# Kernel tuning notes

Measured on AMD Instinct MI355X. Metric: run time of the kernel, lower is better.

Reference implementation:

```python
import jax, jax.numpy as jnp
import numpy as np

HEADS = 8
DIM_HEAD = 64
DIM_INNER = HEADS * DIM_HEAD  # 512
SCALE = DIM_HEAD ** -0.5
B, N, D = 8, 512, 512
NEG = -1e9


def setup_inputs() -> dict:
    key = jax.random.key(0)
    ks = jax.random.split(key, 12)
    inp = {}
    for i in range(3):
        inp[f"x{i}"] = jax.random.normal(ks[i], (B, N, D), dtype=jnp.float32)
        inp[f"m{i}"] = jax.random.randint(ks[3 + i], (B, N), 0, 2).astype(bool)
        inp[f"Wqkv{i}"] = jax.random.normal(ks[6 + i], (D, 3 * DIM_INNER), dtype=jnp.float32) * 0.02
        inp[f"Wout{i}"] = jax.random.normal(ks[9 + i], (DIM_INNER, D), dtype=jnp.float32) * 0.02
    return inp


def _split_heads(t):
    # [b, n, h*d] -> [b, h, n, d]
    b, n, _ = t.shape
    return t.reshape(b, n, HEADS, DIM_HEAD).transpose(0, 2, 1, 3)


def _forward(xs, masks, Wqkvs, Wouts):
    qs, ks, vs = [], [], []
    for x, W in zip(xs, Wqkvs):
        q, k, v = jnp.split(x @ W, 3, axis=-1)
        qs.append(_split_heads(q))
        ks.append(_split_heads(k))
        vs.append(_split_heads(v))
    K = jnp.concatenate(ks, axis=2)  # [b, h, 3n, d]
    V = jnp.concatenate(vs, axis=2)
    outs = []
    for q, m, Wo in zip(qs, masks, Wouts):
        dots = jnp.einsum('bhnd,bhmd->bhnm', q, K) * SCALE
        # original masks whole query rows: masked_fill(~mask[:, None, :, None], -1e9)
        dots = jnp.where(m[:, None, :, None], dots, NEG)
        attn = jax.nn.softmax(dots, axis=-1)  # dropout is identity at eval
        o = jnp.einsum('bhnm,bhmd->bhnd', attn, V)
        o = o.transpose(0, 2, 1, 3).reshape(q.shape[0], q.shape[2], DIM_INNER)
        outs.append(o @ Wo)
    return tuple(outs)


def reference(x0, x1, x2, m0, m1, m2, Wqkv0, Wqkv1, Wqkv2, Wout0, Wout1, Wout2):
    return _forward((x0, x1, x2), (m0, m1, m2), (Wqkv0, Wqkv1, Wqkv2), (Wout0, Wout1, Wout2))
```

## Files before the change

kernel.cpp:

```cpp
#include <hip/hip_runtime.h>
#include <cstdint>
#include <cstddef>

#define NEGV  -1.0e9f
#define QSCALE 0.18033688011112042f

typedef _Float16 h8 __attribute__((ext_vector_type(8)));
typedef _Float16 h4 __attribute__((ext_vector_type(4)));
typedef float    f4 __attribute__((ext_vector_type(4)));


static __device__ inline h8 cvt8(float4 a, float4 b) {
    h8 r = { (_Float16)a.x, (_Float16)a.y, (_Float16)a.z, (_Float16)a.w,
             (_Float16)b.x, (_Float16)b.y, (_Float16)b.z, (_Float16)b.w };
    return r;
}

__global__ __launch_bounds__(256) void wt_cvt(
    const float* __restrict__ q0, const float* __restrict__ q1, const float* __restrict__ q2,
    const float* __restrict__ o0, const float* __restrict__ o1, const float* __restrict__ o2,
    _Float16* __restrict__ Wqt, _Float16* __restrict__ Wot)
{
    const int mod = blockIdx.z;
    const int flat = blockIdx.x;
    const float* s;
    _Float16* d;
    int C, bx, by;
    if (flat < 768) {
        C = 1536; bx = flat % 48; by = flat / 48;
        s = (mod == 0) ? q0 : ((mod == 1) ? q1 : q2);
        d = Wqt + (size_t)mod * 1536 * 512;
    } else {
        C = 512; bx = (flat - 768) % 16; by = (flat - 768) / 16;
        s = (mod == 0) ? o0 : ((mod == 1) ? o1 : o2);
        d = Wot + (size_t)mod * 512 * 512;
    }
    const int c0 = bx * 32, r0 = by * 32;
    __shared__ float tile[32][33];
    const int tr = threadIdx.x >> 3;
    const int tc = (threadIdx.x & 7) * 4;
    float4 v = *reinterpret_cast<const float4*>(&s[(size_t)(r0 + tr) * C + c0 + tc]);
    tile[tr][tc + 0] = v.x; tile[tr][tc + 1] = v.y; tile[tr][tc + 2] = v.z; tile[tr][tc + 3] = v.w;
    __syncthreads();
    h4 o = { (_Float16)tile[tc + 0][tr], (_Float16)tile[tc + 1][tr],
             (_Float16)tile[tc + 2][tr], (_Float16)tile[tc + 3][tr] };
    *reinterpret_cast<h4*>(&d[(size_t)(c0 + tr) * 512 + r0 + tc]) = o;
}

__global__ __launch_bounds__(256) void qkv_gemm_f16(
    const float* __restrict__ x0, const float* __restrict__ x1, const float* __restrict__ x2,
    const _Float16* __restrict__ Wqt,
    _Float16* __restrict__ Qh, _Float16* __restrict__ Kh, _Float16* __restrict__ Vt)
{
    const int mod = blockIdx.z;
    const float* __restrict__ A = (mod == 0) ? x0 : ((mod == 1) ? x1 : x2);
    const _Float16* __restrict__ Bw = Wqt + (size_t)mod * 1536 * 512;

    __shared__ _Float16 smem[2 * 128 * 72];
    _Float16* As = smem;
    _Float16* Bs = smem + 128 * 72;

    const int t = threadIdx.x;
    const int brow = blockIdx.x * 128, bcol = blockIdx.y * 128;
    const int w = t >> 6, l = t & 63;
    const int wr = (w >> 1) * 64, wc = (w & 1) * 64;
    const int lr = l & 15, lg = l >> 4, lk = lg * 8;

    const int sm = t >> 1, sk = (t & 1) * 32;
    const float*    __restrict__ aRow = &A [(size_t)(brow + sm) * 512 + sk];
    const _Float16* __restrict__ bRow = &Bw[(size_t)(bcol + sm) * 512 + sk];
    _Float16* aDst = &As[sm * 72 + sk];
    _Float16* bDst = &Bs[sm * 72 + sk];

    f4 acc[4][4] = {};
    float4 ax[8];
    h8 bx[4];

#pragma unroll
    for (int j = 0; j < 8; j++) ax[j] = *reinterpret_cast<const float4*>(&aRow[j * 4]);
#pragma unroll
    for (int j = 0; j < 4; j++) bx[j] = *reinterpret_cast<const h8*>(&bRow[j * 8]);
#pragma unroll
    for (int j = 0; j < 4; j++) {
        *reinterpret_cast<h8*>(&aDst[j * 8]) = cvt8(ax[2 * j], ax[2 * j + 1]);
        *reinterpret_cast<h8*>(&bDst[j * 8]) = bx[j];
    }

    for (int k0 = 0; k0 < 512; k0 += 64) {
        __syncthreads();
        const bool more = (k0 + 64) < 512;
        if (more) {
            const int kn = k0 + 64;
#pragma unroll
            for (int j = 0; j < 8; j++) ax[j] = *reinterpret_cast<const float4*>(&aRow[kn + j * 4]);
#pragma unroll
            for (int j = 0; j < 4; j++) bx[j] = *reinterpret_cast<const h8*>(&bRow[kn + j * 8]);
        }
#pragma unroll
        for (int ks = 0; ks < 64; ks += 32) {
            h8 af[4], bf[4];
#pragma unroll
            for (int m = 0; m < 4; m++)
                af[m] = *reinterpret_cast<h8*>(&As[(wr + m * 16 + lr) * 72 + ks + lk]);
#pragma unroll
            for (int n = 0; n < 4; n++)
                bf[n] = *reinterpret_cast<h8*>(&Bs[(wc + n * 16 + lr) * 72 + ks + lk]);
            __builtin_amdgcn_s_setprio(1);
#pragma unroll
            for (int m = 0; m < 4; m++)
#pragma unroll
                for (int n = 0; n < 4; n++)
                    acc[m][n] = __builtin_amdgcn_mfma_f32_16x16x32_f16(af[m], bf[n], acc[m][n], 0, 0, 0);
            __builtin_amdgcn_s_setprio(0);
        }
        __syncthreads();
        if (more) {
#pragma unroll
            for (int j = 0; j < 4; j++) {
                *reinterpret_cast<h8*>(&aDst[j * 8]) = cvt8(ax[2 * j], ax[2 * j + 1]);
                *reinterpret_cast<h8*>(&bDst[j * 8]) = bx[j];
            }
        }
    }

    const int sec = bcol >> 9;
    const int b = brow >> 9;
    const int nbase = brow & 511;
    const int cbase = bcol - (sec << 9);

    if (sec == 2) {
#pragma unroll
        for (int m = 0; m < 4; m++) {
            const int n = nbase + wr + m * 16 + lg * 4;
#pragma unroll
            for (int nn = 0; nn < 4; nn++) {
                const int cis = cbase + wc + nn * 16 + lr;
                const int hh = cis >> 6, d = cis & 63;
                h4 pv = { (_Float16)acc[m][nn][0], (_Float16)acc[m][nn][1],
                          (_Float16)acc[m][nn][2], (_Float16)acc[m][nn][3] };
                *reinterpret_cast<h4*>(&Vt[(((size_t)b * 8 + hh) * 64 + d) * 1536 + mod * 512 + n]) = pv;
            }
        }
    } else {
        const float scl = (sec == 0) ? QSCALE : 1.0f;
        _Float16 (*Ts)[136] = reinterpret_cast<_Float16(*)[136]>(smem);
#pragma unroll
        for (int pass = 0; pass < 2; pass++) {
            __syncthreads();
            if ((w >> 1) == pass) {
#pragma unroll
                for (int m = 0; m < 4; m++)
#pragma unroll
                    for (int nn = 0; nn < 4; nn++)
#pragma unroll
                        for (int reg = 0; reg < 4; reg++)
                            Ts[m * 16 + lg * 4 + reg][wc + nn * 16 + lr] =
                                (_Float16)(acc[m][nn][reg] * scl);
            }
            __syncthreads();
#pragma unroll
            for (int it = 0; it < 4; it++) {
                const int idx = t + it * 256;
                const int r = idx >> 4, c = (idx & 15) * 8;
                h8 v = *reinterpret_cast<h8*>(&Ts[r][c]);
                const int n = nbase + pass * 64 + r;
                const int cis = cbase + c;
                const int hh = cis >> 6, d = cis & 63;
                if (sec == 0)
                    *reinterpret_cast<h8*>(&Qh[((((size_t)mod * 8 + b) * 8 + hh) * 512 + n) * 64 + d]) = v;
                else
                    *reinterpret_cast<h8*>(&Kh[(((size_t)b * 8 + hh) * 1536 + mod * 512 + n) * 64 + d]) = v;
            }
        }
    }
}

__global__ __launch_bounds__(512) void attn_f16(
    const _Float16* __restrict__ Qh, const _Float16* __restrict__ Kh, const _Float16* __restrict__ Vt,
    const int* __restrict__ m0, const int* __restrict__ m1, const int* __restrict__ m2,
    _Float16* __restrict__ Oh)
{
    const int mod = blockIdx.z;
    const int bh = blockIdx.x, b = bh >> 3, h = bh & 7;
    const int q0 = blockIdx.y * 128;

    __shared__ _Float16 Ks[64 * 72];
    __shared__ _Float16 Vs[64 * 72];
    __shared__ _Float16 Ps[128 * 72];

    const int t = threadIdx.x, w = t >> 6, l = t & 63;
    const int lr = l & 15, lg = l >> 4, lk = lg * 8;

    const _Float16* __restrict__ Qp = Qh + ((((size_t)mod * 8 + b) * 8 + h) * 512 + q0 + w * 16) * 64;
    h8 qf0 = *reinterpret_cast<const h8*>(&Qp[(size_t)lr * 64 + lk]);
    h8 qf1 = *reinterpret_cast<const h8*>(&Qp[(size_t)lr * 64 + 32 + lk]);

    const int* __restrict__ mk = (mod == 0) ? m0 : ((mod == 1) ? m1 : m2);
    const bool msk = mk[b * 512 + q0 + w * 16 + lr] != 0;

    float mrow = -3.0e38f, lsum = 0.f;
    f4 o[4] = {};

    const int sr = t >> 3, skk = (t & 7) * 8;
    const _Float16* __restrict__ kSrc = Kh + (size_t)bh * 1536 * 64 + (size_t)sr * 64 + skk;
    const _Float16* __restrict__ vSrc = Vt + (size_t)bh * 64 * 1536 + (size_t)sr * 1536 + skk;
    _Float16* kDst = &Ks[sr * 72 + skk];
    _Float16* vDst = &Vs[sr * 72 + skk];

    h8 krg = *reinterpret_cast<const h8*>(kSrc);
    h8 vrg = *reinterpret_cast<const h8*>(vSrc);
    *reinterpret_cast<h8*>(kDst) = krg;
    *reinterpret_cast<h8*>(vDst) = vrg;

    for (int c0 = 0; c0 < 1536; c0 += 64) {
        __syncthreads();
        const bool more = (c0 + 64) < 1536;
        if (more) {
            krg = *reinterpret_cast<const h8*>(kSrc + (size_t)(c0 + 64) * 64);
            vrg = *reinterpret_cast<const h8*>(vSrc + (c0 + 64));
        }

        f4 st[4] = {};
        __builtin_amdgcn_s_setprio(1);
#pragma unroll
        for (int kb = 0; kb < 4; kb++) {
            h8 ka0 = *reinterpret_cast<h8*>(&Ks[(kb * 16 + lr) * 72 + lk]);
            h8 ka1 = *reinterpret_cast<h8*>(&Ks[(kb * 16 + lr) * 72 + 32 + lk]);
            st[kb] = __builtin_amdgcn_mfma_f32_16x16x32_f16(ka0, qf0, st[kb], 0, 0, 0);
            st[kb] = __builtin_amdgcn_mfma_f32_16x16x32_f16(ka1, qf1, st[kb], 0, 0, 0);
        }
        __builtin_amdgcn_s_setprio(0);

        if (!msk) {
#pragma unroll
            for (int kb = 0; kb < 4; kb++) { st[kb][0] = NEGV; st[kb][1] = NEGV; st[kb][2] = NEGV; st[kb][3] = NEGV; }
        }
        float cm = fmaxf(fmaxf(fmaxf(st[0][0], st[0][1]), fmaxf(st[0][2], st[0][3])),
                         fmaxf(fmaxf(st[1][0], st[1][1]), fmaxf(st[1][2], st[1][3])));
        cm = fmaxf(cm, fmaxf(fmaxf(fmaxf(st[2][0], st[2][1]), fmaxf(st[2][2], st[2][3])),
                             fmaxf(fmaxf(st[3][0], st[3][1]), fmaxf(st[3][2], st[3][3]))));
        cm = fmaxf(cm, __shfl_xor(cm, 16));
        cm = fmaxf(cm, __shfl_xor(cm, 32));

        if (!__all(cm <= mrow + 8.0f)) {
            const float mn = fmaxf(mrow, cm);
            const float sc = __builtin_amdgcn_exp2f(mrow - mn);
            mrow = mn;
            lsum *= sc;
#pragma unroll
            for (int dg = 0; dg < 4; dg++) o[dg] *= sc;
        }

        float rs = 0.f;
#pragma unroll
        for (int kb = 0; kb < 4; kb++) {
            const float p0 = __builtin_amdgcn_exp2f(st[kb][0] - mrow);
            const float p1 = __builtin_amdgcn_exp2f(st[kb][1] - mrow);
            const float p2 = __builtin_amdgcn_exp2f(st[kb][2] - mrow);
            const float p3 = __builtin_amdgcn_exp2f(st[kb][3] - mrow);
            rs += (p0 + p1) + (p2 + p3);
            h4 ph = { (_Float16)p0, (_Float16)p1, (_Float16)p2, (_Float16)p3 };
            *reinterpret_cast<h4*>(&Ps[(w * 16 + lr) * 72 + kb * 16 + lg * 4]) = ph;
        }
        rs += __shfl_xor(rs, 16);
        rs += __shfl_xor(rs, 32);
        lsum += rs;

        __builtin_amdgcn_s_setprio(1);
#pragma unroll
        for (int kb2 = 0; kb2 < 2; kb2++) {
            h8 pa = *reinterpret_cast<h8*>(&Ps[(w * 16 + lr) * 72 + kb2 * 32 + lk]);
#pragma unroll
            for (int dg = 0; dg < 4; dg++) {
                h8 va = *reinterpret_cast<h8*>(&Vs[(dg * 16 + lr) * 72 + kb2 * 32 + lk]);
                o[dg] = __builtin_amdgcn_mfma_f32_16x16x32_f16(va, pa, o[dg], 0, 0, 0);
            }
        }
        __builtin_amdgcn_s_setprio(0);

        __syncthreads();
        if (more) {
            *reinterpret_cast<h8*>(kDst) = krg;
            *reinterpret_cast<h8*>(vDst) = vrg;
        }
    }

    const float inv = 1.f / lsum;
    const size_t row = (size_t)mod * 4096 + b * 512 + q0 + w * 16 + lr;
#pragma unroll
    for (int dg = 0; dg < 4; dg++) {
        h4 ov = { (_Float16)(o[dg][0] * inv), (_Float16)(o[dg][1] * inv),
                  (_Float16)(o[dg][2] * inv), (_Float16)(o[dg][3] * inv) };
        *reinterpret_cast<h4*>(&Oh[row * 512 + h * 64 + dg * 16 + lg * 4]) = ov;
    }
}

__global__ __launch_bounds__(256) void out_gemm_f16(
    const _Float16* __restrict__ Oh, const _Float16* __restrict__ Wot,
    float* __restrict__ out)
{
    const int mod = blockIdx.z;
    const _Float16* __restrict__ A  = Oh  + (size_t)mod * 4096 * 512;
    const _Float16* __restrict__ Bw = Wot + (size_t)mod * 512 * 512;
    float* __restrict__ C = out + (size_t)mod * 4096 * 512;

    __shared__ _Float16 smem[(64 + 128) * 72];
    _Float16* As = smem;
    _Float16* Bs = smem + 64 * 72;

    const int t = threadIdx.x;
    const int brow = blockIdx.x * 64, bcol = blockIdx.y * 128;
    const int w = t >> 6, l = t & 63;
    const int wr = (w >> 1) * 32, wc = (w & 1) * 64;
    const int lr = l & 15, lg = l >> 4, lk = lg * 8;

    const int sa = t >> 2, ska = (t & 3) * 16;
    const int sb = t >> 1, skb = (t & 1) * 32;
    const _Float16* __restrict__ aRow = &A [(size_t)(brow + sa) * 512 + ska];
    const _Float16* __restrict__ bRow = &Bw[(size_t)(bcol + sb) * 512 + skb];
    _Float16* aDst = &As[sa * 72 + ska];
    _Float16* bDst = &Bs[sb * 72 + skb];

    f4 acc[2][4] = {};
    h8 axr[2], bxr[4];

#pragma unroll
    for (int j = 0; j < 2; j++) axr[j] = *reinterpret_cast<const h8*>(&aRow[j * 8]);
#pragma unroll
    for (int j = 0; j < 4; j++) bxr[j] = *reinterpret_cast<const h8*>(&bRow[j * 8]);
#pragma unroll
    for (int j = 0; j < 2; j++) *reinterpret_cast<h8*>(&aDst[j * 8]) = axr[j];
#pragma unroll
    for (int j = 0; j < 4; j++) *reinterpret_cast<h8*>(&bDst[j * 8]) = bxr[j];

    for (int k0 = 0; k0 < 512; k0 += 64) {
        __syncthreads();
        const bool more = (k0 + 64) < 512;
        if (more) {
            const int kn = k0 + 64;
#pragma unroll
            for (int j = 0; j < 2; j++) axr[j] = *reinterpret_cast<const h8*>(&aRow[kn + j * 8]);
#pragma unroll
            for (int j = 0; j < 4; j++) bxr[j] = *reinterpret_cast<const h8*>(&bRow[kn + j * 8]);
        }
#pragma unroll
        for (int ks = 0; ks < 64; ks += 32) {
            h8 af[2], bf[4];
#pragma unroll
            for (int m = 0; m < 2; m++)
                af[m] = *reinterpret_cast<h8*>(&As[(wr + m * 16 + lr) * 72 + ks + lk]);
#pragma unroll
            for (int n = 0; n < 4; n++)
                bf[n] = *reinterpret_cast<h8*>(&Bs[(wc + n * 16 + lr) * 72 + ks + lk]);
            __builtin_amdgcn_s_setprio(1);
#pragma unroll
            for (int m = 0; m < 2; m++)
#pragma unroll
                for (int n = 0; n < 4; n++)
                    acc[m][n] = __builtin_amdgcn_mfma_f32_16x16x32_f16(af[m], bf[n], acc[m][n], 0, 0, 0);
            __builtin_amdgcn_s_setprio(0);
        }
        __syncthreads();
        if (more) {
#pragma unroll
            for (int j = 0; j < 2; j++) *reinterpret_cast<h8*>(&aDst[j * 8]) = axr[j];
#pragma unroll
            for (int j = 0; j < 4; j++) *reinterpret_cast<h8*>(&bDst[j * 8]) = bxr[j];
        }
    }

#pragma unroll
    for (int m = 0; m < 2; m++) {
        const int rloc = wr + m * 16 + lg * 4;
#pragma unroll
        for (int reg = 0; reg < 4; reg++) {
            const size_t base = (size_t)(brow + rloc + reg) * 512 + bcol;
#pragma unroll
            for (int nn = 0; nn < 4; nn++)
                C[base + wc + nn * 16 + lr] = acc[m][nn][reg];
        }
    }
}

extern "C" void kernel_launch(void* const* d_in, const int* in_sizes, int n_in,
                              void* d_out, int out_size, void* d_ws, size_t ws_size,
                              hipStream_t stream)
{
    const float* x0  = (const float*)d_in[0];
    const int*   m0  = (const int*)  d_in[1];
    const float* Wq0 = (const float*)d_in[2];
    const float* Wo0 = (const float*)d_in[3];
    const float* x1  = (const float*)d_in[4];
    const int*   m1  = (const int*)  d_in[5];
    const float* Wq1 = (const float*)d_in[6];
    const float* Wo1 = (const float*)d_in[7];
    const float* x2  = (const float*)d_in[8];
    const int*   m2  = (const int*)  d_in[9];
    const float* Wq2 = (const float*)d_in[10];
    const float* Wo2 = (const float*)d_in[11];

    _Float16* Wqt = (_Float16*)d_ws;
    _Float16* Wot = Wqt + 2359296;
    _Float16* Qh  = Wot + 786432;
    _Float16* Kh  = Qh  + 6291456;
    _Float16* Vt  = Kh  + 6291456;
    _Float16* Oh  = Vt  + 6291456;

    wt_cvt<<<dim3(1024, 1, 3), 256, 0, stream>>>(Wq0, Wq1, Wq2, Wo0, Wo1, Wo2, Wqt, Wot);
    qkv_gemm_f16<<<dim3(32, 12, 3), 256, 0, stream>>>(x0, x1, x2, Wqt, Qh, Kh, Vt);
    attn_f16    <<<dim3(64, 4, 3), 512, 0, stream>>>(Qh, Kh, Vt, m0, m1, m2, Oh);
    out_gemm_f16<<<dim3(64, 4, 3), 256, 0, stream>>>(Oh, Wot, (float*)d_out);
}
```

Baseline: 236.3 us.

## Widen attention KV chunk to 128 and rewrite output GEMM as register-only single-wave tiles

The attention kernel now processes 128 keys per iteration instead of 64. This halves the number of barriers and online-softmax rescale checks, at the cost of larger shared buffers for K, V and P. The output projection GEMM drops its shared-memory tiling. It now uses one 64-thread wave per 16x128 output tile, streaming A and B fragments straight from global memory into registers with one-step prefetch. That removes LDS traffic and barriers but loses reuse of B across rows, which raises global/L2 traffic.

```diff
diff --git a/kernel.cpp b/kernel.cpp
--- a/kernel.cpp
+++ b/kernel.cpp
@@ -184,9 +184,9 @@
     const int bh = blockIdx.x, b = bh >> 3, h = bh & 7;
     const int q0 = blockIdx.y * 128;
 
-    __shared__ _Float16 Ks[64 * 72];
-    __shared__ _Float16 Vs[64 * 72];
-    __shared__ _Float16 Ps[128 * 72];
+    __shared__ _Float16 Ks[128 * 72];
+    __shared__ _Float16 Vs[64 * 136];
+    __shared__ _Float16 Ps[128 * 136];
 
     const int t = threadIdx.x, w = t >> 6, l = t & 63;
     const int lr = l & 15, lg = l >> 4, lk = lg * 8;
@@ -202,28 +202,34 @@
     f4 o[4] = {};
 
     const int sr = t >> 3, skk = (t & 7) * 8;
-    const _Float16* __restrict__ kSrc = Kh + (size_t)bh * 1536 * 64 + (size_t)sr * 64 + skk;
-    const _Float16* __restrict__ vSrc = Vt + (size_t)bh * 64 * 1536 + (size_t)sr * 1536 + skk;
-    _Float16* kDst = &Ks[sr * 72 + skk];
-    _Float16* vDst = &Vs[sr * 72 + skk];
-
-    h8 krg = *reinterpret_cast<const h8*>(kSrc);
-    h8 vrg = *reinterpret_cast<const h8*>(vSrc);
-    *reinterpret_cast<h8*>(kDst) = krg;
-    *reinterpret_cast<h8*>(vDst) = vrg;
-
-    for (int c0 = 0; c0 < 1536; c0 += 64) {
+    const _Float16* __restrict__ kSrc = Kh + (size_t)bh * 1536 * 64;
+    const _Float16* __restrict__ vSrc = Vt + (size_t)bh * 64 * 1536 + (size_t)sr * 1536;
+
+    h8 krg[2], vrg[2];
+    krg[0] = *reinterpret_cast<const h8*>(kSrc + (size_t)sr * 64 + skk);
+    krg[1] = *reinterpret_cast<const h8*>(kSrc + (size_t)(sr + 64) * 64 + skk);
+    vrg[0] = *reinterpret_cast<const h8*>(vSrc + skk);
+    vrg[1] = *reinterpret_cast<const h8*>(vSrc + skk + 64);
+    *reinterpret_cast<h8*>(&Ks[sr * 72 + skk]) = krg[0];
+    *reinterpret_cast<h8*>(&Ks[(sr + 64) * 72 + skk]) = krg[1];
+    *reinterpret_cast<h8*>(&Vs[sr * 136 + skk]) = vrg[0];
+    *reinterpret_cast<h8*>(&Vs[sr * 136 + skk + 64]) = vrg[1];
+
+    for (int c0 = 0; c0 < 1536; c0 += 128) {
         __syncthreads();
-        const bool more = (c0 + 64) < 1536;
+        const bool more = (c0 + 128) < 1536;
         if (more) {
-            krg = *reinterpret_cast<const h8*>(kSrc + (size_t)(c0 + 64) * 64);
-            vrg = *reinterpret_cast<const h8*>(vSrc + (c0 + 64));
-        }
-
-        f4 st[4] = {};
+            const int cn = c0 + 128;
+            krg[0] = *reinterpret_cast<const h8*>(kSrc + (size_t)(cn + sr) * 64 + skk);
+            krg[1] = *reinterpret_cast<const h8*>(kSrc + (size_t)(cn + sr + 64) * 64 + skk);
+            vrg[0] = *reinterpret_cast<const h8*>(vSrc + cn + skk);
+            vrg[1] = *reinterpret_cast<const h8*>(vSrc + cn + skk + 64);
+        }
+
+        f4 st[8] = {};
         __builtin_amdgcn_s_setprio(1);
 #pragma unroll
-        for (int kb = 0; kb < 4; kb++) {
+        for (int kb = 0; kb < 8; kb++) {
             h8 ka0 = *reinterpret_cast<h8*>(&Ks[(kb * 16 + lr) * 72 + lk]);
             h8 ka1 = *reinterpret_cast<h8*>(&Ks[(kb * 16 + lr) * 72 + 32 + lk]);
             st[kb] = __builtin_amdgcn_mfma_f32_16x16x32_f16(ka0, qf0, st[kb], 0, 0, 0);
@@ -233,12 +239,12 @@
 
         if (!msk) {
 #pragma unroll
-            for (int kb = 0; kb < 4; kb++) { st[kb][0] = NEGV; st[kb][1] = NEGV; st[kb][2] = NEGV; st[kb][3] = NEGV; }
-        }
-        float cm = fmaxf(fmaxf(fmaxf(st[0][0], st[0][1]), fmaxf(st[0][2], st[0][3])),
-                         fmaxf(fmaxf(st[1][0], st[1][1]), fmaxf(st[1][2], st[1][3])));
-        cm = fmaxf(cm, fmaxf(fmaxf(fmaxf(st[2][0], st[2][1]), fmaxf(st[2][2], st[2][3])),
-                             fmaxf(fmaxf(st[3][0], st[3][1]), fmaxf(st[3][2], st[3][3]))));
+            for (int kb = 0; kb < 8; kb++) { st[kb][0] = NEGV; st[kb][1] = NEGV; st[kb][2] = NEGV; st[kb][3] = NEGV; }
+        }
+        float cm = -3.0e38f;
+#pragma unroll
+        for (int kb = 0; kb < 8; kb++)
+            cm = fmaxf(cm, fmaxf(fmaxf(st[kb][0], st[kb][1]), fmaxf(st[kb][2], st[kb][3])));
         cm = fmaxf(cm, __shfl_xor(cm, 16));
         cm = fmaxf(cm, __shfl_xor(cm, 32));
 
@@ -253,14 +259,14 @@
 
         float rs = 0.f;
 #pragma unroll
-        for (int kb = 0; kb < 4; kb++) {
+        for (int kb = 0; kb < 8; kb++) {
             const float p0 = __builtin_amdgcn_exp2f(st[kb][0] - mrow);
             const float p1 = __builtin_amdgcn_exp2f(st[kb][1] - mrow);
             const float p2 = __builtin_amdgcn_exp2f(st[kb][2] - mrow);
             const float p3 = __builtin_amdgcn_exp2f(st[kb][3] - mrow);
             rs += (p0 + p1) + (p2 + p3);
             h4 ph = { (_Float16)p0, (_Float16)p1, (_Float16)p2, (_Float16)p3 };
-            *reinterpret_cast<h4*>(&Ps[(w * 16 + lr) * 72 + kb * 16 + lg * 4]) = ph;
+            *reinterpret_cast<h4*>(&Ps[(w * 16 + lr) * 136 + kb * 16 + lg * 4]) = ph;
         }
         rs += __shfl_xor(rs, 16);
         rs += __shfl_xor(rs, 32);
@@ -268,11 +274,11 @@
 
         __builtin_amdgcn_s_setprio(1);
 #pragma unroll
-        for (int kb2 = 0; kb2 < 2; kb2++) {
-            h8 pa = *reinterpret_cast<h8*>(&Ps[(w * 16 + lr) * 72 + kb2 * 32 + lk]);
+        for (int kb2 = 0; kb2 < 4; kb2++) {
+            h8 pa = *reinterpret_cast<h8*>(&Ps[(w * 16 + lr) * 136 + kb2 * 32 + lk]);
 #pragma unroll
             for (int dg = 0; dg < 4; dg++) {
-                h8 va = *reinterpret_cast<h8*>(&Vs[(dg * 16 + lr) * 72 + kb2 * 32 + lk]);
+                h8 va = *reinterpret_cast<h8*>(&Vs[(dg * 16 + lr) * 136 + kb2 * 32 + lk]);
                 o[dg] = __builtin_amdgcn_mfma_f32_16x16x32_f16(va, pa, o[dg], 0, 0, 0);
             }
         }
@@ -280,8 +286,10 @@
 
         __syncthreads();
         if (more) {
-            *reinterpret_cast<h8*>(kDst) = krg;
-            *reinterpret_cast<h8*>(vDst) = vrg;
+            *reinterpret_cast<h8*>(&Ks[sr * 72 + skk]) = krg[0];
+            *reinterpret_cast<h8*>(&Ks[(sr + 64) * 72 + skk]) = krg[1];
+            *reinterpret_cast<h8*>(&Vs[sr * 136 + skk]) = vrg[0];
+            *reinterpret_cast<h8*>(&Vs[sr * 136 + skk + 64]) = vrg[1];
         }
     }
 
@@ -295,91 +303,45 @@
     }
 }
 
-__global__ __launch_bounds__(256) void out_gemm_f16(
+__global__ __launch_bounds__(64) void out_gemm_f16(
     const _Float16* __restrict__ Oh, const _Float16* __restrict__ Wot,
     float* __restrict__ out)
 {
-    const int mod = blockIdx.z;
-    const _Float16* __restrict__ A  = Oh  + (size_t)mod * 4096 * 512;
-    const _Float16* __restrict__ Bw = Wot + (size_t)mod * 512 * 512;
-    float* __restrict__ C = out + (size_t)mod * 4096 * 512;
-
-    __shared__ _Float16 smem[(64 + 128) * 72];
-    _Float16* As = smem;
-    _Float16* Bs = smem + 64 * 72;
-
-    const int t = threadIdx.x;
-    const int brow = blockIdx.x * 64, bcol = blockIdx.y * 128;
-    const int w = t >> 6, l = t & 63;
-    const int wr = (w >> 1) * 32, wc = (w & 1) * 64;
-    const int lr = l & 15, lg = l >> 4, lk = lg * 8;
-
-    const int sa = t >> 2, ska = (t & 3) * 16;
-    const int sb = t >> 1, skb = (t & 1) * 32;
-    const _Float16* __restrict__ aRow = &A [(size_t)(brow + sa) * 512 + ska];
-    const _Float16* __restrict__ bRow = &Bw[(size_t)(bcol + sb) * 512 + skb];
-    _Float16* aDst = &As[sa * 72 + ska];
-    _Float16* bDst = &Bs[sb * 72 + skb];
-
-    f4 acc[2][4] = {};
-    h8 axr[2], bxr[4];
-
-#pragma unroll
-    for (int j = 0; j < 2; j++) axr[j] = *reinterpret_cast<const h8*>(&aRow[j * 8]);
-#pragma unroll
-    for (int j = 0; j < 4; j++) bxr[j] = *reinterpret_cast<const h8*>(&bRow[j * 8]);
-#pragma unroll
-    for (int j = 0; j < 2; j++) *reinterpret_cast<h8*>(&aDst[j * 8]) = axr[j];
-#pragma unroll
-    for (int j = 0; j < 4; j++) *reinterpret_cast<h8*>(&bDst[j * 8]) = bxr[j];
-
-    for (int k0 = 0; k0 < 512; k0 += 64) {
-        __syncthreads();
-        const bool more = (k0 + 64) < 512;
-        if (more) {
-            const int kn = k0 + 64;
-#pragma unroll
-            for (int j = 0; j < 2; j++) axr[j] = *reinterpret_cast<const h8*>(&aRow[kn + j * 8]);
-#pragma unroll
-            for (int j = 0; j < 4; j++) bxr[j] = *reinterpret_cast<const h8*>(&bRow[kn + j * 8]);
-        }
-#pragma unroll
-        for (int ks = 0; ks < 64; ks += 32) {
-            h8 af[2], bf[4];
-#pragma unroll
-            for (int m = 0; m < 2; m++)
-                af[m] = *reinterpret_cast<h8*>(&As[(wr + m * 16 + lr) * 72 + ks + lk]);
-#pragma unroll
-            for (int n = 0; n < 4; n++)
-                bf[n] = *reinterpret_cast<h8*>(&Bs[(wc + n * 16 + lr) * 72 + ks + lk]);
-            __builtin_amdgcn_s_setprio(1);
-#pragma unroll
-            for (int m = 0; m < 2; m++)
-#pragma unroll
-                for (int n = 0; n < 4; n++)
-                    acc[m][n] = __builtin_amdgcn_mfma_f32_16x16x32_f16(af[m], bf[n], acc[m][n], 0, 0, 0);
-            __builtin_amdgcn_s_setprio(0);
-        }
-        __syncthreads();
-        if (more) {
-#pragma unroll
-            for (int j = 0; j < 2; j++) *reinterpret_cast<h8*>(&aDst[j * 8]) = axr[j];
-#pragma unroll
-            for (int j = 0; j < 4; j++) *reinterpret_cast<h8*>(&bDst[j * 8]) = bxr[j];
-        }
-    }
-
-#pragma unroll
-    for (int m = 0; m < 2; m++) {
-        const int rloc = wr + m * 16 + lg * 4;
-#pragma unroll
-        for (int reg = 0; reg < 4; reg++) {
-            const size_t base = (size_t)(brow + rloc + reg) * 512 + bcol;
-#pragma unroll
-            for (int nn = 0; nn < 4; nn++)
-                C[base + wc + nn * 16 + lr] = acc[m][nn][reg];
-        }
-    }
+    const int mod = blockIdx.z, rg = blockIdx.y, cc = blockIdx.x;
+    const _Float16* __restrict__ Ap = Oh  + ((size_t)mod * 4096 + rg * 16) * 512;
+    const _Float16* __restrict__ Bp = Wot + (size_t)mod * 512 * 512 + (size_t)cc * 128 * 512;
+    float* __restrict__ C = out + ((size_t)mod * 4096 + rg * 16) * 512 + cc * 128;
+
+    const int l = threadIdx.x, lr = l & 15, lg = l >> 4;
+
+    f4 acc[8] = {};
+    h8 bcur[8], bnxt[8];
+#pragma unroll
+    for (int cb = 0; cb < 8; cb++)
+        bcur[cb] = *reinterpret_cast<const h8*>(&Bp[(size_t)(cb * 16 + lr) * 512 + lg * 8]);
+
+#pragma unroll
+    for (int ks = 0; ks < 16; ks++) {
+        const h8 a = *reinterpret_cast<const h8*>(&Ap[(size_t)lr * 512 + ks * 32 + lg * 8]);
+        if (ks < 15) {
+#pragma unroll
+            for (int cb = 0; cb < 8; cb++)
+                bnxt[cb] = *reinterpret_cast<const h8*>(&Bp[(size_t)(cb * 16 + lr) * 512 + (ks + 1) * 32 + lg * 8]);
+        }
+        __builtin_amdgcn_s_setprio(1);
+#pragma unroll
+        for (int cb = 0; cb < 8; cb++)
+            acc[cb] = __builtin_amdgcn_mfma_f32_16x16x32_f16(a, bcur[cb], acc[cb], 0, 0, 0);
+        __builtin_amdgcn_s_setprio(0);
+#pragma unroll
+        for (int cb = 0; cb < 8; cb++) bcur[cb] = bnxt[cb];
+    }
+
+#pragma unroll
+    for (int cb = 0; cb < 8; cb++)
+#pragma unroll
+        for (int reg = 0; reg < 4; reg++)
+            C[(size_t)(lg * 4 + reg) * 512 + cb * 16 + lr] = acc[cb][reg];
 }
 
 extern "C" void kernel_launch(void* const* d_in, const int* in_sizes, int n_in,
@@ -409,5 +371,5 @@
     wt_cvt<<<dim3(1024, 1, 3), 256, 0, stream>>>(Wq0, Wq1, Wq2, Wo0, Wo1, Wo2, Wqt, Wot);
     qkv_gemm_f16<<<dim3(32, 12, 3), 256, 0, stream>>>(x0, x1, x2, Wqt, Qh, Kh, Vt);
     attn_f16    <<<dim3(64, 4, 3), 512, 0, stream>>>(Qh, Kh, Vt, m0, m1, m2, Oh);
-    out_gemm_f16<<<dim3(64, 4, 3), 256, 0, stream>>>(Oh, Wot, (float*)d_out);
-}
+    out_gemm_f16<<<dim3(4, 256, 3), 64, 0, stream>>>(Oh, Wot, (float*)d_out);
+}
```

Result: slower. 277.3 us (+17.3%).

## Restructure attention to 32x32 MFMA with register-resident K and P

Applied to the files above, without the earlier changes.

Rewrites the attention kernel so each wave handles 64 query rows with 32x32x16 MFMAs instead of 16 rows with 16x16x32. K fragments are loaded directly from global memory into registers with one-step prefetch, dropping the K shared tile. The softmax probabilities are packed and exchanged through cross-lane shuffles instead of a shared P buffer, and V goes into an XOR-swizzled unpadded shared tile. Blocks shrink to 128 threads, which lowers block-level parallelism and raises register pressure per thread in exchange for fewer LDS round trips and more work per MFMA.

```diff
diff --git a/kernel.cpp b/kernel.cpp
--- a/kernel.cpp
+++ b/kernel.cpp
@@ -7,7 +7,10 @@
 
 typedef _Float16 h8 __attribute__((ext_vector_type(8)));
 typedef _Float16 h4 __attribute__((ext_vector_type(4)));
+typedef _Float16 h2 __attribute__((ext_vector_type(2)));
 typedef float    f4 __attribute__((ext_vector_type(4)));
+typedef float    f16x __attribute__((ext_vector_type(16)));
+typedef unsigned int u32x4 __attribute__((ext_vector_type(4)));
 
 
 static __device__ inline h8 cvt8(float4 a, float4 b) {
@@ -175,7 +178,7 @@
     }
 }
 
-__global__ __launch_bounds__(512) void attn_f16(
+__global__ __launch_bounds__(128) void attn_f16(
     const _Float16* __restrict__ Qh, const _Float16* __restrict__ Kh, const _Float16* __restrict__ Vt,
     const int* __restrict__ m0, const int* __restrict__ m1, const int* __restrict__ m2,
     _Float16* __restrict__ Oh)
@@ -184,114 +187,166 @@
     const int bh = blockIdx.x, b = bh >> 3, h = bh & 7;
     const int q0 = blockIdx.y * 128;
 
-    __shared__ _Float16 Ks[64 * 72];
-    __shared__ _Float16 Vs[64 * 72];
-    __shared__ _Float16 Ps[128 * 72];
+    __shared__ _Float16 Vs[64 * 64];
 
     const int t = threadIdx.x, w = t >> 6, l = t & 63;
-    const int lr = l & 15, lg = l >> 4, lk = lg * 8;
-
-    const _Float16* __restrict__ Qp = Qh + ((((size_t)mod * 8 + b) * 8 + h) * 512 + q0 + w * 16) * 64;
-    h8 qf0 = *reinterpret_cast<const h8*>(&Qp[(size_t)lr * 64 + lk]);
-    h8 qf1 = *reinterpret_cast<const h8*>(&Qp[(size_t)lr * 64 + 32 + lk]);
+    const int r = l & 31, hi = l >> 5;
+
+    const _Float16* __restrict__ Qp = Qh + ((((size_t)mod * 8 + b) * 8 + h) * 512 + q0 + w * 64) * 64;
+    h8 qf[2][4];
+#pragma unroll
+    for (int qb = 0; qb < 2; qb++)
+#pragma unroll
+        for (int dk = 0; dk < 4; dk++)
+            qf[qb][dk] = *reinterpret_cast<const h8*>(&Qp[(size_t)(qb * 32 + r) * 64 + dk * 16 + hi * 8]);
 
     const int* __restrict__ mk = (mod == 0) ? m0 : ((mod == 1) ? m1 : m2);
-    const bool msk = mk[b * 512 + q0 + w * 16 + lr] != 0;
-
-    float mrow = -3.0e38f, lsum = 0.f;
-    f4 o[4] = {};
-
-    const int sr = t >> 3, skk = (t & 7) * 8;
-    const _Float16* __restrict__ kSrc = Kh + (size_t)bh * 1536 * 64 + (size_t)sr * 64 + skk;
-    const _Float16* __restrict__ vSrc = Vt + (size_t)bh * 64 * 1536 + (size_t)sr * 1536 + skk;
-    _Float16* kDst = &Ks[sr * 72 + skk];
-    _Float16* vDst = &Vs[sr * 72 + skk];
-
-    h8 krg = *reinterpret_cast<const h8*>(kSrc);
-    h8 vrg = *reinterpret_cast<const h8*>(vSrc);
-    *reinterpret_cast<h8*>(kDst) = krg;
-    *reinterpret_cast<h8*>(vDst) = vrg;
+    bool msk[2];
+#pragma unroll
+    for (int qb = 0; qb < 2; qb++)
+        msk[qb] = mk[b * 512 + q0 + w * 64 + qb * 32 + r] != 0;
+
+    float mrow[2] = { -3.0e38f, -3.0e38f };
+    float lsum[2] = { 0.f, 0.f };
+    f16x o[2][2] = {};
+
+    const _Float16* __restrict__ Kp = Kh + (size_t)bh * 1536 * 64;
+    const _Float16* __restrict__ Vp = Vt + (size_t)bh * 64 * 1536;
+
+    const int vr = t >> 1, vs4 = (t & 1) * 4;
+    h8 vrg[4];
+#pragma unroll
+    for (int j = 0; j < 4; j++)
+        vrg[j] = *reinterpret_cast<const h8*>(&Vp[(size_t)vr * 1536 + (vs4 + j) * 8]);
+#pragma unroll
+    for (int j = 0; j < 4; j++)
+        *reinterpret_cast<h8*>(&Vs[vr * 64 + (((vs4 + j) ^ (vr & 7)) * 8)]) = vrg[j];
+
+    h8 kn[4];
+#pragma unroll
+    for (int dk = 0; dk < 4; dk++)
+        kn[dk] = *reinterpret_cast<const h8*>(&Kp[(size_t)r * 64 + dk * 16 + hi * 8]);
 
     for (int c0 = 0; c0 < 1536; c0 += 64) {
         __syncthreads();
         const bool more = (c0 + 64) < 1536;
         if (more) {
-            krg = *reinterpret_cast<const h8*>(kSrc + (size_t)(c0 + 64) * 64);
-            vrg = *reinterpret_cast<const h8*>(vSrc + (c0 + 64));
-        }
-
-        f4 st[4] = {};
-        __builtin_amdgcn_s_setprio(1);
-#pragma unroll
-        for (int kb = 0; kb < 4; kb++) {
-            h8 ka0 = *reinterpret_cast<h8*>(&Ks[(kb * 16 + lr) * 72 + lk]);
-            h8 ka1 = *reinterpret_cast<h8*>(&Ks[(kb * 16 + lr) * 72 + 32 + lk]);
-            st[kb] = __builtin_amdgcn_mfma_f32_16x16x32_f16(ka0, qf0, st[kb], 0, 0, 0);
-            st[kb] = __builtin_amdgcn_mfma_f32_16x16x32_f16(ka1, qf1, st[kb], 0, 0, 0);
-        }
-        __builtin_amdgcn_s_setprio(0);
-
-        if (!msk) {
-#pragma unroll
-            for (int kb = 0; kb < 4; kb++) { st[kb][0] = NEGV; st[kb][1] = NEGV; st[kb][2] = NEGV; st[kb][3] = NEGV; }
-        }
-        float cm = fmaxf(fmaxf(fmaxf(st[0][0], st[0][1]), fmaxf(st[0][2], st[0][3])),
-                         fmaxf(fmaxf(st[1][0], st[1][1]), fmaxf(st[1][2], st[1][3])));
-        cm = fmaxf(cm, fmaxf(fmaxf(fmaxf(st[2][0], st[2][1]), fmaxf(st[2][2], st[2][3])),
-                             fmaxf(fmaxf(st[3][0], st[3][1]), fmaxf(st[3][2], st[3][3]))));
-        cm = fmaxf(cm, __shfl_xor(cm, 16));
-        cm = fmaxf(cm, __shfl_xor(cm, 32));
-
-        if (!__all(cm <= mrow + 8.0f)) {
-            const float mn = fmaxf(mrow, cm);
-            const float sc = __builtin_amdgcn_exp2f(mrow - mn);
-            mrow = mn;
-            lsum *= sc;
-#pragma unroll
-            for (int dg = 0; dg < 4; dg++) o[dg] *= sc;
-        }
-
-        float rs = 0.f;
-#pragma unroll
-        for (int kb = 0; kb < 4; kb++) {
-            const float p0 = __builtin_amdgcn_exp2f(st[kb][0] - mrow);
-            const float p1 = __builtin_amdgcn_exp2f(st[kb][1] - mrow);
-            const float p2 = __builtin_amdgcn_exp2f(st[kb][2] - mrow);
-            const float p3 = __builtin_amdgcn_exp2f(st[kb][3] - mrow);
-            rs += (p0 + p1) + (p2 + p3);
-            h4 ph = { (_Float16)p0, (_Float16)p1, (_Float16)p2, (_Float16)p3 };
-            *reinterpret_cast<h4*>(&Ps[(w * 16 + lr) * 72 + kb * 16 + lg * 4]) = ph;
-        }
-        rs += __shfl_xor(rs, 16);
-        rs += __shfl_xor(rs, 32);
-        lsum += rs;
-
-        __builtin_amdgcn_s_setprio(1);
-#pragma unroll
-        for (int kb2 = 0; kb2 < 2; kb2++) {
-            h8 pa = *reinterpret_cast<h8*>(&Ps[(w * 16 + lr) * 72 + kb2 * 32 + lk]);
-#pragma unroll
-            for (int dg = 0; dg < 4; dg++) {
-                h8 va = *reinterpret_cast<h8*>(&Vs[(dg * 16 + lr) * 72 + kb2 * 32 + lk]);
-                o[dg] = __builtin_amdgcn_mfma_f32_16x16x32_f16(va, pa, o[dg], 0, 0, 0);
-            }
-        }
-        __builtin_amdgcn_s_setprio(0);
-
-        __syncthreads();
-        if (more) {
-            *reinterpret_cast<h8*>(kDst) = krg;
-            *reinterpret_cast<h8*>(vDst) = vrg;
-        }
-    }
-
-    const float inv = 1.f / lsum;
-    const size_t row = (size_t)mod * 4096 + b * 512 + q0 + w * 16 + lr;
-#pragma unroll
-    for (int dg = 0; dg < 4; dg++) {
-        h4 ov = { (_Float16)(o[dg][0] * inv), (_Float16)(o[dg][1] * inv),
-                  (_Float16)(o[dg][2] * inv), (_Float16)(o[dg][3] * inv) };
-        *reinterpret_cast<h4*>(&Oh[row * 512 + h * 64 + dg * 16 + lg * 4]) = ov;
+#pragma unroll
+            for (int j = 0; j < 4; j++)
+                vrg[j] = *reinterpret_cast<const h8*>(&Vp[(size_t)vr * 1536 + c0 + 64 + (vs4 + j) * 8]);
+        }
+
+#pragma unroll
+        for (int s32 = 0; s32 < 2; s32++) {
+            h8 kc[4];
+#pragma unroll
+            for (int dk = 0; dk < 4; dk++) kc[dk] = kn[dk];
+            if (s32 == 0 || more) {
+                const int nc = (s32 == 0) ? (c0 + 32) : (c0 + 64);
+#pragma unroll
+                for (int dk = 0; dk < 4; dk++)
+                    kn[dk] = *reinterpret_cast<const h8*>(&Kp[(size_t)(nc + r) * 64 + dk * 16 + hi * 8]);
+            }
+
+            f16x st[2] = {};
+            __builtin_amdgcn_s_setprio(1);
+#pragma unroll
+            for (int dk = 0; dk < 4; dk++) {
+                st[0] = __builtin_amdgcn_mfma_f32_32x32x16_f16(kc[dk], qf[0][dk], st[0], 0, 0, 0);
+                st[1] = __builtin_amdgcn_mfma_f32_32x32x16_f16(kc[dk], qf[1][dk], st[1], 0, 0, 0);
+            }
+            __builtin_amdgcn_s_setprio(0);
+
+            u32x4 pbw[2][2];
+#pragma unroll
+            for (int qb = 0; qb < 2; qb++) {
+                if (!msk[qb]) {
+#pragma unroll
+                    for (int reg = 0; reg < 16; reg++) st[qb][reg] = NEGV;
+                }
+                float cm = st[qb][0];
+#pragma unroll
+                for (int reg = 1; reg < 16; reg++) cm = fmaxf(cm, st[qb][reg]);
+                cm = fmaxf(cm, __shfl_xor(cm, 32));
+
+                if (!__all(cm <= mrow[qb] + 8.0f)) {
+                    const float mn = fmaxf(mrow[qb], cm);
+                    const float sc = __builtin_amdgcn_exp2f(mrow[qb] - mn);
+                    mrow[qb] = mn;
+                    lsum[qb] *= sc;
+                    o[qb][0] *= sc;
+                    o[qb][1] *= sc;
+                }
+
+                float p[16];
+                float rs = 0.f;
+#pragma unroll
+                for (int reg = 0; reg < 16; reg++) {
+                    p[reg] = __builtin_amdgcn_exp2f(st[qb][reg] - mrow[qb]);
+                    rs += p[reg];
+                }
+                rs += __shfl_xor(rs, 32);
+                lsum[qb] += rs;
+
+#pragma unroll
+                for (int kk = 0; kk < 2; kk++) {
+                    unsigned int a0 = __builtin_bit_cast(unsigned int,
+                        __builtin_amdgcn_cvt_pkrtz(p[8 * kk + 0], p[8 * kk + 1]));
+                    unsigned int a1 = __builtin_bit_cast(unsigned int,
+                        __builtin_amdgcn_cvt_pkrtz(p[8 * kk + 2], p[8 * kk + 3]));
+                    unsigned int b0 = __builtin_bit_cast(unsigned int,
+                        __builtin_amdgcn_cvt_pkrtz(p[8 * kk + 4], p[8 * kk + 5]));
+                    unsigned int b1 = __builtin_bit_cast(unsigned int,
+                        __builtin_amdgcn_cvt_pkrtz(p[8 * kk + 6], p[8 * kk + 7]));
+                    const unsigned int ra0 = __shfl_xor(a0, 32);
+                    const unsigned int ra1 = __shfl_xor(a1, 32);
+                    const unsigned int rb0 = __shfl_xor(b0, 32);
+                    const unsigned int rb1 = __shfl_xor(b1, 32);
+                    u32x4 pw;
+                    if (hi == 0) { pw[0] = a0; pw[1] = a1; pw[2] = ra0; pw[3] = ra1; }
+                    else         { pw[0] = rb0; pw[1] = rb1; pw[2] = b0; pw[3] = b1; }
+                    pbw[qb][kk] = pw;
+                }
+            }
+
+            __builtin_amdgcn_s_setprio(1);
+#pragma unroll
+            for (int kk = 0; kk < 2; kk++) {
+                const h8 pb0 = __builtin_bit_cast(h8, pbw[0][kk]);
+                const h8 pb1 = __builtin_bit_cast(h8, pbw[1][kk]);
+#pragma unroll
+                for (int dg = 0; dg < 2; dg++) {
+                    h8 va = *reinterpret_cast<h8*>(
+                        &Vs[(dg * 32 + r) * 64 + (((s32 * 4 + kk * 2 + hi) ^ (r & 7)) * 8)]);
+                    o[0][dg] = __builtin_amdgcn_mfma_f32_32x32x16_f16(va, pb0, o[0][dg], 0, 0, 0);
+                    o[1][dg] = __builtin_amdgcn_mfma_f32_32x32x16_f16(va, pb1, o[1][dg], 0, 0, 0);
+                }
+            }
+            __builtin_amdgcn_s_setprio(0);
+        }
+
+        __syncthreads();
+        if (more) {
+#pragma unroll
+            for (int j = 0; j < 4; j++)
+                *reinterpret_cast<h8*>(&Vs[vr * 64 + (((vs4 + j) ^ (vr & 7)) * 8)]) = vrg[j];
+        }
+    }
+
+#pragma unroll
+    for (int qb = 0; qb < 2; qb++) {
+        const float inv = 1.f / lsum[qb];
+        const size_t row = (size_t)mod * 4096 + b * 512 + q0 + w * 64 + qb * 32 + r;
+#pragma unroll
+        for (int dg = 0; dg < 2; dg++)
+#pragma unroll
+            for (int a = 0; a < 4; a++) {
+                h4 ov = { (_Float16)(o[qb][dg][4 * a + 0] * inv),
+                          (_Float16)(o[qb][dg][4 * a + 1] * inv),
+                          (_Float16)(o[qb][dg][4 * a + 2] * inv),
+                          (_Float16)(o[qb][dg][4 * a + 3] * inv) };
+                *reinterpret_cast<h4*>(&Oh[row * 512 + h * 64 + dg * 32 + a * 8 + hi * 4]) = ov;
+            }
     }
 }
 
@@ -408,6 +463,6 @@
 
     wt_cvt<<<dim3(1024, 1, 3), 256, 0, stream>>>(Wq0, Wq1, Wq2, Wo0, Wo1, Wo2, Wqt, Wot);
     qkv_gemm_f16<<<dim3(32, 12, 3), 256, 0, stream>>>(x0, x1, x2, Wqt, Qh, Kh, Vt);
-    attn_f16    <<<dim3(64, 4, 3), 512, 0, stream>>>(Qh, Kh, Vt, m0, m1, m2, Oh);
+    attn_f16    <<<dim3(64, 4, 3), 128, 0, stream>>>(Qh, Kh, Vt, m0, m1, m2, Oh);
     out_gemm_f16<<<dim3(64, 4, 3), 256, 0, stream>>>(Oh, Wot, (float*)d_out);
 }
```

After: 302.9 us. +28.2%, slower.
